# Kernel tuning notes

Measured on AMD Instinct MI355X. Metric: run time of the kernel, lower is better.

The kernel has to match this reference:

```python
import jax, jax.numpy as jnp
import numpy as np

DT = 0.01  # hard-coded timestep in _tt_floquet_forward_tf
OMEGA = 1.0  # drive_frequency default


def setup_inputs() -> dict:
    key = jax.random.key(0)
    k1, k2, k3, k4 = jax.random.split(key, 4)
    B, S, D, M = 4, 4096, 4096, 16
    x = jax.random.normal(k1, (B, S, D), dtype=jnp.float32)
    floquet_energies = jax.random.normal(k2, (M, D), dtype=jnp.float32) * 0.01  # RandomNormal(stddev=0.01)
    drive_weights = jax.random.normal(k3, (M,), dtype=jnp.float32)
    coupling_matrix = jax.random.normal(k4, (M, M), dtype=jnp.float32)
    return {
        "x": x,
        "floquet_energies": floquet_energies,
        "drive_weights": drive_weights,
        "coupling_matrix": coupling_matrix,
    }


def reference(x, floquet_energies, drive_weights, coupling_matrix):
    # Per the TF fallback, per timestep t:
    #   z_n = x_t * exp(-i n w t)                      (demodulate into Floquet modes)
    #   z_n <- z_n * exp(-i eps_n dt)                  (quasi-energy rotation)
    #   y_t = Re( sum_n z_n * exp(+i n w (t+dt)) )     (remodulate at t+dt)
    # The n*w*t phase cancels, leaving a time-independent per-dim gain:
    #   y[t,d] = x[t,d] * sum_n cos(n*w*dt - eps[n,d]*dt)
    # with eps[n,d] = floquet_energies[n,d] * (1 + 0.1 * drive_weights[n]).
    # coupling_matrix is unused by the fallback forward.
    modes = floquet_energies.shape[0]
    n = jnp.arange(modes, dtype=x.dtype)                                  # [M]
    eps = floquet_energies * (1.0 + 0.1 * drive_weights)[:, None]         # [M, D]
    coef = jnp.cos(n[:, None] * (OMEGA * DT) - eps * DT)                  # [M, D]
    gain = jnp.sum(coef, axis=0)                                          # [D]
    return x * gain  # [B, S, D]
```

## Files before the change

### kernel.cpp

```cpp
#include <hip/hip_runtime.h>


#define F_DT 0.01f
#define F_OMEGA 1.0f

typedef float f32x4 __attribute__((ext_vector_type(4)));

__global__ __launch_bounds__(1024) void fused_rows_kernel(
        const f32x4* __restrict__ x4,
        const f32x4* __restrict__ fe4,
        const float* __restrict__ dw,
        f32x4* __restrict__ out4,
        int M, int Dq, long long n4) {
    const int t = threadIdx.x;

    f32x4 g = {0.0f, 0.0f, 0.0f, 0.0f};
    #pragma unroll 4
    for (int n = 0; n < M; ++n) {
        f32x4 e = fe4[(long long)n * Dq + t];
        float w = (1.0f + 0.1f * dw[n]) * F_DT;
        float a = (float)n * (F_OMEGA * F_DT);
        g.x += cosf(a - e.x * w);
        g.y += cosf(a - e.y * w);
        g.z += cosf(a - e.z * w);
        g.w += cosf(a - e.w * w);
    }

    const long long stride = (long long)gridDim.x * Dq;
    for (long long i = (long long)blockIdx.x * Dq + t; i < n4; i += stride) {
        f32x4 xv = __builtin_nontemporal_load(&x4[i]);
        f32x4 o = xv * g;
        __builtin_nontemporal_store(o, &out4[i]);
    }
}

__global__ void fused_scalar_kernel(
        const float* __restrict__ x,
        const float* __restrict__ fe,
        const float* __restrict__ dw,
        float* __restrict__ out,
        int M, int D, long long n) {
    const long long stride = (long long)gridDim.x * blockDim.x;
    for (long long i = (long long)blockIdx.x * blockDim.x + threadIdx.x;
         i < n; i += stride) {
        int d = (int)(i % D);
        float g = 0.0f;
        for (int nn = 0; nn < M; ++nn) {
            float eps = fe[(long long)nn * D + d] * (1.0f + 0.1f * dw[nn]);
            g += cosf((float)nn * (F_OMEGA * F_DT) - eps * F_DT);
        }
        out[i] = x[i] * g;
    }
}

extern "C" void kernel_launch(void* const* d_in, const int* in_sizes, int n_in,
                              void* d_out, int out_size, void* d_ws, size_t ws_size,
                              hipStream_t stream) {
    const float* x  = (const float*)d_in[0];
    const float* fe = (const float*)d_in[1];
    const float* dw = (const float*)d_in[2];

    float* out = (float*)d_out;
    (void)d_ws; (void)ws_size;

    int M = in_sizes[2];
    int D = in_sizes[1] / M;
    long long n = (long long)in_sizes[0];

    const int Dq = D / 4;
    const bool vec_ok = (D % 4 == 0) && (n % D == 0) &&
                        (Dq >= 64) && (Dq <= 1024) && (Dq % 64 == 0);

    if (vec_ok) {
        long long n4 = n / 4;
        long long rows = n4 / Dq;
        int blocks = (int)(rows < 2048 ? rows : 2048);
        fused_rows_kernel<<<blocks, Dq, 0, stream>>>(
            (const f32x4*)x, (const f32x4*)fe, dw, (f32x4*)out, M, Dq, n4);
    } else {
        int threads = 256;
        long long want = (n + threads - 1) / threads;
        int blocks = (int)(want < 2048 ? want : 2048);
        fused_scalar_kernel<<<blocks, threads, 0, stream>>>(
            x, fe, dw, out, M, D, n);
    }
}
```

Measured before the change: 484.2 us.

## Split gain computation into separate kernel and drop nontemporal loads/stores

Computes the per-dimension gain once in a small dedicated kernel that writes to workspace, then runs a streaming scale kernel that loads the precomputed gain instead of recomputing 16 cosines per block. This removes the redundant gain computation repeated in each of the 2048 blocks, at the cost of an extra kernel launch and a dependency through global memory. The streaming loop also switches from nontemporal loads and stores to plain ones, which changes how the cache treats the large x and out streams.

```diff
diff --git a/kernel.cpp b/kernel.cpp
--- a/kernel.cpp
+++ b/kernel.cpp
@@ -6,16 +6,12 @@
 
 typedef float f32x4 __attribute__((ext_vector_type(4)));
 
-__global__ __launch_bounds__(1024) void fused_rows_kernel(
-        const f32x4* __restrict__ x4,
-        const f32x4* __restrict__ fe4,
-        const float* __restrict__ dw,
-        f32x4* __restrict__ out4,
-        int M, int Dq, long long n4) {
-    const int t = threadIdx.x;
-
+__global__ void gain_kernel_v4(const f32x4* __restrict__ fe4,
+                               const float* __restrict__ dw,
+                               f32x4* __restrict__ gain4, int M, int Dq) {
+    int t = blockIdx.x * blockDim.x + threadIdx.x;
+    if (t >= Dq) return;
     f32x4 g = {0.0f, 0.0f, 0.0f, 0.0f};
-    #pragma unroll 4
     for (int n = 0; n < M; ++n) {
         f32x4 e = fe4[(long long)n * Dq + t];
         float w = (1.0f + 0.1f * dw[n]) * F_DT;
@@ -25,31 +21,43 @@
         g.z += cosf(a - e.z * w);
         g.w += cosf(a - e.w * w);
     }
+    gain4[t] = g;
+}
 
+__global__ __launch_bounds__(1024) void scale_rows_kernel(
+        const f32x4* __restrict__ x4,
+        const f32x4* __restrict__ gain4,
+        f32x4* __restrict__ out4,
+        int Dq, long long n4) {
+    const int t = threadIdx.x;
+    const f32x4 g = gain4[t];
     const long long stride = (long long)gridDim.x * Dq;
     for (long long i = (long long)blockIdx.x * Dq + t; i < n4; i += stride) {
-        f32x4 xv = __builtin_nontemporal_load(&x4[i]);
-        f32x4 o = xv * g;
-        __builtin_nontemporal_store(o, &out4[i]);
+        out4[i] = x4[i] * g;
     }
 }
 
-__global__ void fused_scalar_kernel(
-        const float* __restrict__ x,
-        const float* __restrict__ fe,
-        const float* __restrict__ dw,
-        float* __restrict__ out,
-        int M, int D, long long n) {
+__global__ void gain_kernel_scalar(const float* __restrict__ fe,
+                                   const float* __restrict__ dw,
+                                   float* __restrict__ gain, int M, int D) {
+    int d = blockIdx.x * blockDim.x + threadIdx.x;
+    if (d >= D) return;
+    float g = 0.0f;
+    for (int n = 0; n < M; ++n) {
+        float eps = fe[(long long)n * D + d] * (1.0f + 0.1f * dw[n]);
+        g += cosf((float)n * (F_OMEGA * F_DT) - eps * F_DT);
+    }
+    gain[d] = g;
+}
+
+__global__ void scale_kernel_scalar(const float* __restrict__ x,
+                                    const float* __restrict__ gain,
+                                    float* __restrict__ out,
+                                    int D, long long n) {
     const long long stride = (long long)gridDim.x * blockDim.x;
     for (long long i = (long long)blockIdx.x * blockDim.x + threadIdx.x;
          i < n; i += stride) {
-        int d = (int)(i % D);
-        float g = 0.0f;
-        for (int nn = 0; nn < M; ++nn) {
-            float eps = fe[(long long)nn * D + d] * (1.0f + 0.1f * dw[nn]);
-            g += cosf((float)nn * (F_OMEGA * F_DT) - eps * F_DT);
-        }
-        out[i] = x[i] * g;
+        out[i] = x[i] * gain[(int)(i % D)];
     }
 }
 
@@ -60,8 +68,8 @@
     const float* fe = (const float*)d_in[1];
     const float* dw = (const float*)d_in[2];
 
-    float* out = (float*)d_out;
-    (void)d_ws; (void)ws_size;
+    float* out  = (float*)d_out;
+    float* gain = (float*)d_ws;
 
     int M = in_sizes[2];
     int D = in_sizes[1] / M;
@@ -72,16 +80,30 @@
                         (Dq >= 64) && (Dq <= 1024) && (Dq % 64 == 0);
 
     if (vec_ok) {
-        long long n4 = n / 4;
-        long long rows = n4 / Dq;
-        int blocks = (int)(rows < 2048 ? rows : 2048);
-        fused_rows_kernel<<<blocks, Dq, 0, stream>>>(
-            (const f32x4*)x, (const f32x4*)fe, dw, (f32x4*)out, M, Dq, n4);
+        {
+            int threads = 256;
+            int blocks = (Dq + threads - 1) / threads;
+            gain_kernel_v4<<<blocks, threads, 0, stream>>>(
+                (const f32x4*)fe, dw, (f32x4*)gain, M, Dq);
+        }
+        {
+            long long n4 = n / 4;
+            long long rows = n4 / Dq;
+            int blocks = (int)(rows < 2048 ? rows : 2048);
+            scale_rows_kernel<<<blocks, Dq, 0, stream>>>(
+                (const f32x4*)x, (const f32x4*)gain, (f32x4*)out, Dq, n4);
+        }
     } else {
-        int threads = 256;
-        long long want = (n + threads - 1) / threads;
-        int blocks = (int)(want < 2048 ? want : 2048);
-        fused_scalar_kernel<<<blocks, threads, 0, stream>>>(
-            x, fe, dw, out, M, D, n);
+        {
+            int threads = 256;
+            int blocks = (D + threads - 1) / threads;
+            gain_kernel_scalar<<<blocks, threads, 0, stream>>>(fe, dw, gain, M, D);
+        }
+        {
+            int threads = 256;
+            long long want = (n + threads - 1) / threads;
+            int blocks = (int)(want < 2048 ? want : 2048);
+            scale_kernel_scalar<<<blocks, threads, 0, stream>>>(x, gain, out, D, n);
+        }
     }
 }
```

New measurement: 450.2 us. -7.0%, faster.
